# Kernel tuning notes

Measured on AMD Instinct MI355X. Metric: run time of the kernel, lower is better.

The kernel has to match this reference:

```python
import jax, jax.numpy as jnp
import numpy as np


def setup_inputs() -> dict:
    key = jax.random.key(0)
    k1, k2, k3, k4, k5 = jax.random.split(key, 5)
    N, M, K = 200000, 50, 4
    T = 1000.0
    ti = jnp.sort(jax.random.uniform(k1, (N,), dtype=jnp.float32) * T)
    mi = jax.random.randint(k2, (N,), 0, M, dtype=jnp.int64)
    mu_at_events = jax.random.uniform(k3, (N,), dtype=jnp.float32) * 0.5 + 0.05
    alpha = jax.random.uniform(k4, (K, M, M), dtype=jnp.float32) * 0.1
    gamma = jax.random.uniform(k5, (K,), dtype=jnp.float32) * 2.0 + 0.5
    return {"ti": ti, "mi": mi, "mu_at_events": mu_at_events, "alpha": alpha, "gamma": gamma}


def _hawkes_logsum(ti, mi, mu_at_events, alpha, gamma):
    # ti: [N] sorted event times; mi: [N] event types in [0, M)
    # alpha: [K, M, M]; gamma: [K]; mu_at_events: [N]
    N = ti.shape[0]
    M = alpha.shape[1]
    # inter-event gaps; dt[0] = 0 so the first event has zero excitation state
    dt = jnp.concatenate([jnp.zeros((1,), ti.dtype), ti[1:] - ti[:-1]])  # [N]
    a = jnp.exp(-gamma[None, :] * dt[:, None])  # [N, K] decay factors
    # one-hot of the PREVIOUS event's type (row 0 is all-zero, matching e_mi)
    prev_onehot = jnp.zeros((N, M), ti.dtype).at[jnp.arange(1, N), mi[:-1]].set(1.0)
    b = a[:, None, :] * prev_onehot[:, :, None]  # [N, M, K]

    # linear recurrence S_i = a_i * S_{i-1} + b_i via associative scan
    # combine((a1,b1),(a2,b2)) = (a1*a2, a2*b1 + b2)
    def combine(x, y):
        a1, b1 = x
        a2, b2 = y
        return (a1 * a2, a2[:, None, :] * b1 + b2)

    _, S = jax.lax.associative_scan(combine, (a, b))  # S: [N, M, K]
    # S[i, m, k] = sum_{j < i, m_j = m} exp(-gamma_k (t_i - t_j))
    alpha_at = alpha[:, mi, :]  # [K, N, M] rows of alpha for each event's type
    lam = mu_at_events + jnp.einsum('knm,nmk,k->n', alpha_at, S, gamma)  # [N]
    return jnp.sum(jnp.log(lam))


def reference(ti, mi, mu_at_events, alpha, gamma):
    return _hawkes_logsum(ti, mi, mu_at_events, alpha, gamma)
```

## Files before the change

### kernel.cpp

```cpp
#include <hip/hip_runtime.h>

#define CHUNK 256
#define MM 50
#define KK 4
#define STATE 200
#define ASTRIDE 51
#define SUP 32
#define NSMAX 26
#define GMAX 1024

__device__ int   g_ticket;
__device__ float g_chunkB[GMAX * STATE];
__device__ float g_superB[64 * STATE];

__device__ __forceinline__ unsigned short f2bf(float x) {
  unsigned u = __float_as_uint(x);
  u += 0x7fffu + ((u >> 16) & 1u);
  return (unsigned short)(u >> 16);
}
__device__ __forceinline__ float bflo(unsigned u) { return __uint_as_float(u << 16); }
__device__ __forceinline__ float bfhi(unsigned u) { return __uint_as_float(u & 0xffff0000u); }

__device__ __forceinline__ void st_agent(float* p, float v) {
  __hip_atomic_store(p, v, __ATOMIC_RELAXED, __HIP_MEMORY_SCOPE_AGENT);
}
__device__ __forceinline__ float ld_agent(const float* p) {
  return __hip_atomic_load(p, __ATOMIC_RELAXED, __HIP_MEMORY_SCOPE_AGENT);
}

__global__ __launch_bounds__(512) void hawkes_df(
    const float* __restrict__ ti, const int* __restrict__ mi,
    const float* __restrict__ mu, const float* __restrict__ alpha,
    const float* __restrict__ gamma, float* __restrict__ out,
    int N, int G, int NB) {
  int tid = threadIdx.x;
  __shared__ int vid_s;
  __shared__ unsigned P0[MM * ASTRIDE];
  __shared__ unsigned P1[MM * ASTRIDE];
  __shared__ __align__(16) float4 Fj[512];
  __shared__ int   cj[512];
  __shared__ __align__(16) float Q[16][STATE];
  __shared__ float SB1[STATE];
  __shared__ float SB2[STATE];
  __shared__ float teL[SUP];
  __shared__ float tlast[NSMAX];
  __shared__ float red8[8];

  if (tid == 0) vid_s = atomicAdd(&g_ticket, 1);

  int b = blockIdx.x;
  int c0 = 2 * b;
  int lQ = c0 * CHUNK;
  int sup = b >> 4;
  int g0c = sup * SUP;
  int nloc = c0 - g0c;
  int ch = tid >> 8;

  float gk0 = gamma[0], gk1 = gamma[1], gk2 = gamma[2], gk3 = gamma[3];

  for (int i = tid; i < 16 * STATE; i += 512) ((float*)Q)[i] = 0.f;
  if (tid < SUP) {
    int c = g0c + tid;
    if (c < G) teL[tid] = ti[min(N, (c + 1) * CHUNK) - 1];
  } else if (tid >= 64 && tid < 64 + NSMAX) {
    int s = tid - 64;
    if (s < sup) tlast[s] = ti[min(N, (s + 1) * SUP * CHUNK) - 1];
  }
  if (b == 0 && tid == 0) st_agent(out, 0.f);

  float tref0 = ti[(b == 0) ? 0 : (lQ - 1)];
  float tref_ch = ch ? ti[min(N - 1, lQ + CHUNK - 1)] : tref0;
  int n = lQ + tid;
  bool has_n = (n < N);
  float ti_n = has_n ? ti[n] : 0.f;
  int   mi_n = has_n ? mi[n] : 0;
  float mu_n = has_n ? mu[n] : 0.f;
  int j = lQ - 1 + tid;
  float ti_j = __shfl_up(ti_n, 1, 64);
  int   mi_j = __shfl_up(mi_n, 1, 64);
  if ((tid & 63) == 0 && j >= 0) { ti_j = ti[j]; mi_j = mi[j]; }
  bool valid = (j >= 0) && has_n;
  int myc = valid ? mi_j : 0;
  float4 F = make_float4(0.f, 0.f, 0.f, 0.f);
  if (valid) {
    float tj = ti_j - tref_ch;
    F = make_float4(__expf(gk0 * tj), __expf(gk1 * tj),
                    __expf(gk2 * tj), __expf(gk3 * tj));
  }
  cj[tid] = myc;
  Fj[tid] = F;
  __syncthreads();

  if (valid) {
    float* q = &Q[tid >> 5][myc * KK];
    atomicAdd(q + 0, F.x); atomicAdd(q + 1, F.y);
    atomicAdd(q + 2, F.z); atomicAdd(q + 3, F.w);
  }
  #pragma unroll
  for (int u = 0; u < 5; ++u) {
    int idx = tid + 512 * u;
    if (idx < MM * MM) {
      int c = idx / MM, cp = idx - c * MM;
      float a0 = gk0 * alpha[idx];
      float a1 = gk1 * alpha[2500 + idx];
      float a2 = gk2 * alpha[5000 + idx];
      float a3 = gk3 * alpha[7500 + idx];
      P0[c * ASTRIDE + cp] = (unsigned)f2bf(a0) | ((unsigned)f2bf(a1) << 16);
      P1[c * ASTRIDE + cp] = (unsigned)f2bf(a2) | ((unsigned)f2bf(a3) << 16);
    }
  }
  __syncthreads();

  float epoch_s = ((vid_s / NB) & 1) ? -1.f : 1.f;
  float gkc = (tid & 2) ? ((tid & 1) ? gk3 : gk2) : ((tid & 1) ? gk1 : gk0);
  float totA = 0.f, totB = 0.f, dA = 0.f, dB = 0.f;
  if (tid < STATE) {
    #pragma unroll
    for (int q = 0; q < 8; ++q)  totA += Q[q][tid];
    #pragma unroll
    for (int q = 8; q < 16; ++q) totB += Q[q][tid];
    dA = __expf(-gkc * (teL[nloc] - tref0));
    dB = __expf(-gkc * (teL[nloc + 1] - teL[nloc]));
    st_agent(&g_chunkB[(size_t)c0 * STATE + tid], epoch_s * (dA * totA + 1.f));
    st_agent(&g_chunkB[(size_t)(c0 + 1) * STATE + tid], epoch_s * (dB * totB + 1.f));
  }

  float4 acc = make_float4(0.f, 0.f, 0.f, 0.f);
  if (has_n) {
    int rowb = mi_n * ASTRIDE;
    int base = tid & ~31;
    #pragma unroll 4
    for (int s = base; s <= tid; ++s) {
      unsigned p0 = P0[rowb + cj[s]];
      unsigned p1 = P1[rowb + cj[s]];
      float4 f = Fj[s];
      acc.x += bflo(p0) * f.x; acc.y += bfhi(p0) * f.y;
      acc.z += bflo(p1) * f.z; acc.w += bfhi(p1) * f.w;
    }
  }

  bool closer = ((b & 15) == 15) || (b == NB - 1);
  bool grpA = (tid < STATE);
  bool grpB = (tid >= 256) && (tid < 256 + STATE);
  int st = grpB ? (tid - 256) : tid;
  float SA = 0.f;

  int cpar = nloc >> 1;
  if (grpA && cpar) {
    float r[15];
    #pragma unroll
    for (int i = 0; i < 15; ++i)
      r[i] = (i < cpar) ? ld_agent(&g_chunkB[(size_t)(g0c + 2 * i) * STATE + st]) : epoch_s;
    #pragma unroll
    for (int i = 0; i < 15; ++i) if (i < cpar) {
      float v = r[i];
      while (epoch_s * v < 0.5f) {
        __builtin_amdgcn_s_sleep(1);
        v = ld_agent(&g_chunkB[(size_t)(g0c + 2 * i) * STATE + st]);
      }
      SA += __expf(-gkc * (tref0 - teL[2 * i])) * (epoch_s * v - 1.f);
    }
  }
  if (grpB) {
    float PB = 0.f;
    if (cpar) {
      float r[15];
      #pragma unroll
      for (int i = 0; i < 15; ++i)
        r[i] = (i < cpar) ? ld_agent(&g_chunkB[(size_t)(g0c + 2 * i + 1) * STATE + st]) : epoch_s;
      #pragma unroll
      for (int i = 0; i < 15; ++i) if (i < cpar) {
        float v = r[i];
        while (epoch_s * v < 0.5f) {
          __builtin_amdgcn_s_sleep(1);
          v = ld_agent(&g_chunkB[(size_t)(g0c + 2 * i + 1) * STATE + st]);
        }
        PB += __expf(-gkc * (tref0 - teL[2 * i + 1])) * (epoch_s * v - 1.f);
      }
    }
    SB1[st] = PB;
  }

  if (closer) {
    __syncthreads();
    if (grpA) {
      float Sin = SA + SB1[st];
      float run2 = dA * (Sin + totA);
      run2 = dB * (run2 + totB);
      st_agent(&g_superB[(size_t)sup * STATE + st], epoch_s * (run2 + 1.f));
      SA = Sin;
    }
  }

  int cse = (sup + 1) >> 1, cso = sup >> 1;
  if (grpA && cse) {
    float r[13];
    #pragma unroll
    for (int i = 0; i < 13; ++i)
      r[i] = (i < cse) ? ld_agent(&g_superB[(size_t)(2 * i) * STATE + st]) : epoch_s;
    #pragma unroll
    for (int i = 0; i < 13; ++i) if (i < cse) {
      float v = r[i];
      while (epoch_s * v < 0.5f) {
        __builtin_amdgcn_s_sleep(1);
        v = ld_agent(&g_superB[(size_t)(2 * i) * STATE + st]);
      }
      SA += __expf(-gkc * (tref0 - tlast[2 * i])) * (epoch_s * v - 1.f);
    }
  }
  if (grpB) {
    float PB2 = 0.f;
    if (cso) {
      float r[12];
      #pragma unroll
      for (int i = 0; i < 12; ++i)
        r[i] = (i < cso) ? ld_agent(&g_superB[(size_t)(2 * i + 1) * STATE + st]) : epoch_s;
      #pragma unroll
      for (int i = 0; i < 12; ++i) if (i < cso) {
        float v = r[i];
        while (epoch_s * v < 0.5f) {
          __builtin_amdgcn_s_sleep(1);
          v = ld_agent(&g_superB[(size_t)(2 * i + 1) * STATE + st]);
        }
        PB2 += __expf(-gkc * (tref0 - tlast[2 * i + 1])) * (epoch_s * v - 1.f);
      }
    }
    SB2[st] = PB2;
  }
  __syncthreads();

  if (grpA) {
    float S = SA + SB2[st] + (closer ? 0.f : SB1[st]);
    float run = S;
    #pragma unroll
    for (int q = 0; q < 8; ++q)  { float t = Q[q][st]; Q[q][st] = run; run += t; }
    run = dA * run;
    #pragma unroll
    for (int q = 8; q < 16; ++q) { float t = Q[q][st]; Q[q][st] = run; run += t; }
  }
  __syncthreads();

  float local = 0.f;
  if (has_n) {
    int rowb = mi_n * ASTRIDE;
    const float4* wb = (const float4*)&Q[tid >> 5][0];
    #pragma unroll 10
    for (int m = 0; m < MM; ++m) {
      unsigned p0 = P0[rowb + m];
      unsigned p1 = P1[rowb + m];
      float4 w = wb[m];
      acc.x += bflo(p0) * w.x; acc.y += bfhi(p0) * w.y;
      acc.z += bflo(p1) * w.z; acc.w += bfhi(p1) * w.w;
    }
    float tn = ti_n - tref_ch;
    float lam = mu_n
              + __expf(-gk0 * tn) * acc.x + __expf(-gk1 * tn) * acc.y
              + __expf(-gk2 * tn) * acc.z + __expf(-gk3 * tn) * acc.w;
    local = __logf(lam);
  }
  #pragma unroll
  for (int off = 32; off > 0; off >>= 1)
    local += __shfl_down(local, off, 64);
  if ((tid & 63) == 0) red8[tid >> 6] = local;
  __syncthreads();
  if (tid == 0) {
    float acc8 = 0.f;
    #pragma unroll
    for (int w = 0; w < 8; ++w) acc8 += red8[w];
    atomicAdd(out, acc8);
  }
}

extern "C" void kernel_launch(void* const* d_in, const int* in_sizes, int n_in,
                              void* d_out, int out_size, void* d_ws, size_t ws_size,
                              hipStream_t stream) {
  const float* ti    = (const float*)d_in[0];
  const int*   mi    = (const int*)d_in[1];
  const float* mu    = (const float*)d_in[2];
  const float* alpha = (const float*)d_in[3];
  const float* gamma = (const float*)d_in[4];
  float* out = (float*)d_out;
  int N = in_sizes[0];
  int G = (N + CHUNK - 1) / CHUNK;
  if (G > GMAX) return;
  int NB = (G + 1) / 2;

  hawkes_df<<<NB, 512, 0, stream>>>(ti, mi, mu, alpha, gamma, out, N, G, NB);
}
```

Baseline: 85.86 us.

## Split each event across two threads and parallelize super-chunk prefix loads

Result: slower. 101.2 us (+17.9%).

```diff
diff --git a/kernel.cpp b/kernel.cpp
--- a/kernel.cpp
+++ b/kernel.cpp
@@ -28,7 +28,7 @@
   return __hip_atomic_load(p, __ATOMIC_RELAXED, __HIP_MEMORY_SCOPE_AGENT);
 }
 
-__global__ __launch_bounds__(512) void hawkes_df(
+__global__ __launch_bounds__(1024) void hawkes_df2(
     const float* __restrict__ ti, const int* __restrict__ mi,
     const float* __restrict__ mu, const float* __restrict__ alpha,
     const float* __restrict__ gamma, float* __restrict__ out,
@@ -42,9 +42,10 @@
   __shared__ __align__(16) float Q[16][STATE];
   __shared__ float SB1[STATE];
   __shared__ float SB2[STATE];
+  __shared__ float SB3[STATE];
   __shared__ float teL[SUP];
   __shared__ float tlast[NSMAX];
-  __shared__ float red8[8];
+  __shared__ float red16[16];
 
   if (tid == 0) vid_s = atomicAdd(&g_ticket, 1);
 
@@ -54,11 +55,13 @@
   int sup = b >> 4;
   int g0c = sup * SUP;
   int nloc = c0 - g0c;
-  int ch = tid >> 8;
+  int e = tid >> 1;
+  int h = tid & 1;
+  int ch = e >> 8;
 
   float gk0 = gamma[0], gk1 = gamma[1], gk2 = gamma[2], gk3 = gamma[3];
 
-  for (int i = tid; i < 16 * STATE; i += 512) ((float*)Q)[i] = 0.f;
+  for (int i = tid; i < 16 * STATE; i += 1024) ((float*)Q)[i] = 0.f;
   if (tid < SUP) {
     int c = g0c + tid;
     if (c < G) teL[tid] = ti[min(N, (c + 1) * CHUNK) - 1];
@@ -70,35 +73,34 @@
 
   float tref0 = ti[(b == 0) ? 0 : (lQ - 1)];
   float tref_ch = ch ? ti[min(N - 1, lQ + CHUNK - 1)] : tref0;
-  int n = lQ + tid;
+  int n = lQ + e;
   bool has_n = (n < N);
   float ti_n = has_n ? ti[n] : 0.f;
   int   mi_n = has_n ? mi[n] : 0;
   float mu_n = has_n ? mu[n] : 0.f;
-  int j = lQ - 1 + tid;
-  float ti_j = __shfl_up(ti_n, 1, 64);
-  int   mi_j = __shfl_up(mi_n, 1, 64);
-  if ((tid & 63) == 0 && j >= 0) { ti_j = ti[j]; mi_j = mi[j]; }
+  int j = n - 1;
+  float ti_j = __shfl_up(ti_n, 2, 64);
+  int   mi_j = __shfl_up(mi_n, 2, 64);
+  if ((tid & 63) < 2 && j >= 0) { ti_j = ti[j]; mi_j = mi[j]; }
   bool valid = (j >= 0) && has_n;
   int myc = valid ? mi_j : 0;
-  float4 F = make_float4(0.f, 0.f, 0.f, 0.f);
+  float ga = h ? gk2 : gk0, gb = h ? gk3 : gk1;
+  float2 F2 = make_float2(0.f, 0.f);
   if (valid) {
     float tj = ti_j - tref_ch;
-    F = make_float4(__expf(gk0 * tj), __expf(gk1 * tj),
-                    __expf(gk2 * tj), __expf(gk3 * tj));
-  }
-  cj[tid] = myc;
-  Fj[tid] = F;
+    F2 = make_float2(__expf(ga * tj), __expf(gb * tj));
+  }
+  if (h == 0) cj[e] = myc;
+  ((float2*)&Fj[e])[h] = F2;
   __syncthreads();
 
   if (valid) {
-    float* q = &Q[tid >> 5][myc * KK];
-    atomicAdd(q + 0, F.x); atomicAdd(q + 1, F.y);
-    atomicAdd(q + 2, F.z); atomicAdd(q + 3, F.w);
+    float* q = &Q[e >> 5][myc * KK + 2 * h];
+    atomicAdd(q + 0, F2.x); atomicAdd(q + 1, F2.y);
   }
   #pragma unroll
-  for (int u = 0; u < 5; ++u) {
-    int idx = tid + 512 * u;
+  for (int u = 0; u < 3; ++u) {
+    int idx = tid + 1024 * u;
     if (idx < MM * MM) {
       int c = idx / MM, cp = idx - c * MM;
       float a0 = gk0 * alpha[idx];
@@ -126,11 +128,11 @@
   }
 
   float4 acc = make_float4(0.f, 0.f, 0.f, 0.f);
+  int rowb = mi_n * ASTRIDE;
   if (has_n) {
-    int rowb = mi_n * ASTRIDE;
-    int base = tid & ~31;
+    int base = e & ~31;
     #pragma unroll 4
-    for (int s = base; s <= tid; ++s) {
+    for (int s = base + h; s <= e; s += 2) {
       unsigned p0 = P0[rowb + cj[s]];
       unsigned p1 = P1[rowb + cj[s]];
       float4 f = Fj[s];
@@ -142,10 +144,13 @@
   bool closer = ((b & 15) == 15) || (b == NB - 1);
   bool grpA = (tid < STATE);
   bool grpB = (tid >= 256) && (tid < 256 + STATE);
-  int st = grpB ? (tid - 256) : tid;
+  bool grpC = (tid >= 512) && (tid < 512 + STATE);
+  bool grpD = (tid >= 768) && (tid < 768 + STATE);
+  int st = tid & 255;
   float SA = 0.f;
-
   int cpar = nloc >> 1;
+  int cse = (sup + 1) >> 1, cso = sup >> 1;
+
   if (grpA && cpar) {
     float r[15];
     #pragma unroll
@@ -180,6 +185,44 @@
     }
     SB1[st] = PB;
   }
+  if (grpC) {
+    float PC = 0.f;
+    if (cse) {
+      float r[13];
+      #pragma unroll
+      for (int i = 0; i < 13; ++i)
+        r[i] = (i < cse) ? ld_agent(&g_superB[(size_t)(2 * i) * STATE + st]) : epoch_s;
+      #pragma unroll
+      for (int i = 0; i < 13; ++i) if (i < cse) {
+        float v = r[i];
+        while (epoch_s * v < 0.5f) {
+          __builtin_amdgcn_s_sleep(1);
+          v = ld_agent(&g_superB[(size_t)(2 * i) * STATE + st]);
+        }
+        PC += __expf(-gkc * (tref0 - tlast[2 * i])) * (epoch_s * v - 1.f);
+      }
+    }
+    SB2[st] = PC;
+  }
+  if (grpD) {
+    float PD = 0.f;
+    if (cso) {
+      float r[12];
+      #pragma unroll
+      for (int i = 0; i < 12; ++i)
+        r[i] = (i < cso) ? ld_agent(&g_superB[(size_t)(2 * i + 1) * STATE + st]) : epoch_s;
+      #pragma unroll
+      for (int i = 0; i < 12; ++i) if (i < cso) {
+        float v = r[i];
+        while (epoch_s * v < 0.5f) {
+          __builtin_amdgcn_s_sleep(1);
+          v = ld_agent(&g_superB[(size_t)(2 * i + 1) * STATE + st]);
+        }
+        PD += __expf(-gkc * (tref0 - tlast[2 * i + 1])) * (epoch_s * v - 1.f);
+      }
+    }
+    SB3[st] = PD;
+  }
 
   if (closer) {
     __syncthreads();
@@ -191,46 +234,10 @@
       SA = Sin;
     }
   }
-
-  int cse = (sup + 1) >> 1, cso = sup >> 1;
-  if (grpA && cse) {
-    float r[13];
-    #pragma unroll
-    for (int i = 0; i < 13; ++i)
-      r[i] = (i < cse) ? ld_agent(&g_superB[(size_t)(2 * i) * STATE + st]) : epoch_s;
-    #pragma unroll
-    for (int i = 0; i < 13; ++i) if (i < cse) {
-      float v = r[i];
-      while (epoch_s * v < 0.5f) {
-        __builtin_amdgcn_s_sleep(1);
-        v = ld_agent(&g_superB[(size_t)(2 * i) * STATE + st]);
-      }
-      SA += __expf(-gkc * (tref0 - tlast[2 * i])) * (epoch_s * v - 1.f);
-    }
-  }
-  if (grpB) {
-    float PB2 = 0.f;
-    if (cso) {
-      float r[12];
-      #pragma unroll
-      for (int i = 0; i < 12; ++i)
-        r[i] = (i < cso) ? ld_agent(&g_superB[(size_t)(2 * i + 1) * STATE + st]) : epoch_s;
-      #pragma unroll
-      for (int i = 0; i < 12; ++i) if (i < cso) {
-        float v = r[i];
-        while (epoch_s * v < 0.5f) {
-          __builtin_amdgcn_s_sleep(1);
-          v = ld_agent(&g_superB[(size_t)(2 * i + 1) * STATE + st]);
-        }
-        PB2 += __expf(-gkc * (tref0 - tlast[2 * i + 1])) * (epoch_s * v - 1.f);
-      }
-    }
-    SB2[st] = PB2;
-  }
   __syncthreads();
 
   if (grpA) {
-    float S = SA + SB2[st] + (closer ? 0.f : SB1[st]);
+    float S = SA + SB2[st] + SB3[st] + (closer ? 0.f : SB1[st]);
     float run = S;
     #pragma unroll
     for (int q = 0; q < 8; ++q)  { float t = Q[q][st]; Q[q][st] = run; run += t; }
@@ -242,16 +249,22 @@
 
   float local = 0.f;
   if (has_n) {
-    int rowb = mi_n * ASTRIDE;
-    const float4* wb = (const float4*)&Q[tid >> 5][0];
-    #pragma unroll 10
-    for (int m = 0; m < MM; ++m) {
+    const float4* wb = (const float4*)&Q[e >> 5][0];
+    int mlo = h * 25, mhi = mlo + 25;
+    #pragma unroll 5
+    for (int m = mlo; m < mhi; ++m) {
       unsigned p0 = P0[rowb + m];
       unsigned p1 = P1[rowb + m];
       float4 w = wb[m];
       acc.x += bflo(p0) * w.x; acc.y += bfhi(p0) * w.y;
       acc.z += bflo(p1) * w.z; acc.w += bfhi(p1) * w.w;
     }
+  }
+  acc.x += __shfl_xor(acc.x, 1, 64);
+  acc.y += __shfl_xor(acc.y, 1, 64);
+  acc.z += __shfl_xor(acc.z, 1, 64);
+  acc.w += __shfl_xor(acc.w, 1, 64);
+  if (h == 0 && has_n) {
     float tn = ti_n - tref_ch;
     float lam = mu_n
               + __expf(-gk0 * tn) * acc.x + __expf(-gk1 * tn) * acc.y
@@ -261,13 +274,13 @@
   #pragma unroll
   for (int off = 32; off > 0; off >>= 1)
     local += __shfl_down(local, off, 64);
-  if ((tid & 63) == 0) red8[tid >> 6] = local;
+  if ((tid & 63) == 0) red16[tid >> 6] = local;
   __syncthreads();
   if (tid == 0) {
-    float acc8 = 0.f;
-    #pragma unroll
-    for (int w = 0; w < 8; ++w) acc8 += red8[w];
-    atomicAdd(out, acc8);
+    float acc16 = 0.f;
+    #pragma unroll
+    for (int w = 0; w < 16; ++w) acc16 += red16[w];
+    atomicAdd(out, acc16);
   }
 }
 
@@ -285,5 +298,5 @@
   if (G > GMAX) return;
   int NB = (G + 1) / 2;
 
-  hawkes_df<<<NB, 512, 0, stream>>>(ti, mi, mu, alpha, gamma, out, N, G, NB);
-}
+  hawkes_df2<<<NB, 1024, 0, stream>>>(ti, mi, mu, alpha, gamma, out, N, G, NB);
+}
```
